# Optimization experiments

Hardware: AMD Instinct MI355X
Metric: run time of the kernel (lower is better)

Reference implementation:

```python
import jax, jax.numpy as jnp
import numpy as np
from jax import lax

C = 768
CA = C // 4  # adapter_channels = 192
L = 197      # 1 CLS + 14*14 patches
T_FRAMES = 16
B = 16
N = B * T_FRAMES


def quick_gelu(x):
    return x * jax.nn.sigmoid(1.702 * x)


def setup_inputs() -> dict:
    key = jax.random.key(0)
    ks = jax.random.split(key, 16)
    s = 0.02
    return {
        "x": jax.random.normal(ks[0], (L, N, C), dtype=jnp.float32),
        "T": T_FRAMES,
        # main path (fc1 -> depthwise conv1d over T -> fc2)
        "fc1_w": jax.random.normal(ks[1], (C, CA), jnp.float32) * s,
        "fc1_b": jnp.zeros((CA,), jnp.float32),
        "conv_w": jax.random.normal(ks[2], (CA, 1, 3), jnp.float32) * s,  # (O, I/g, K)
        "conv_b": jnp.zeros((CA,), jnp.float32),
        "fc2_w": jax.random.normal(ks[3], (CA, C), jnp.float32) * s,
        "fc2_b": jnp.zeros((C,), jnp.float32),
        # offset adapter (fc1 -> depthwise conv3d (1,3,3) -> fc2)
        "off_fc1_w": jax.random.normal(ks[4], (C, CA), jnp.float32) * s,
        "off_fc1_b": jnp.zeros((CA,), jnp.float32),
        "off_conv_w": jax.random.normal(ks[5], (CA, 1, 1, 3, 3), jnp.float32) * s,  # (O, I/g, D, H, W)
        "off_conv_b": jnp.zeros((CA,), jnp.float32),
        "off_fc2_w": jax.random.normal(ks[6], (CA, C), jnp.float32) * s,
        "off_fc2_b": jnp.zeros((C,), jnp.float32),
        # mlp branch (c_in -> QuickGELU -> c_out)
        "mlp_in_w": jax.random.normal(ks[7], (C, CA), jnp.float32) * s,
        "mlp_in_b": jnp.zeros((CA,), jnp.float32),
        "mlp_out_w": jax.random.normal(ks[8], (CA, C), jnp.float32) * s,
        "mlp_out_b": jnp.zeros((C,), jnp.float32),
    }


def _offset_adapter(x, T, fc1_w, fc1_b, conv_w, conv_b, fc2_w, fc2_b):
    Lx, Nx, Cx = x.shape
    Bx = Nx // T
    HW = Lx - 1
    H = int(round(HW ** 0.5))
    Ca = fc1_w.shape[1]
    xp = jnp.transpose(x, (1, 0, 2))            # (N, L, C)
    xs = xp[:, 1:, :].reshape(Bx, T, HW, Cx)    # (B, T, HW, C)
    # former frame: index [0, 0, 1, ..., T-2]
    x_former = jnp.concatenate([xs[:, :1], xs[:, :-1]], axis=1)
    off = xs - x_former
    off = off @ fc1_w + fc1_b                   # (B, T, HW, Ca)
    off = off.reshape(Bx, T, H, H, Ca).transpose(0, 4, 1, 2, 3)  # (B, Ca, T, H, W)
    off = lax.conv_general_dilated(
        off, conv_w, window_strides=(1, 1, 1),
        padding=[(0, 0), (1, 1), (1, 1)],
        dimension_numbers=("NCDHW", "OIDHW", "NCDHW"),
        feature_group_count=Ca,
    ) + conv_b[None, :, None, None, None]
    off = off.transpose(0, 2, 3, 4, 1).reshape(Nx, HW, Ca)
    off = off @ fc2_w + fc2_b                   # (N, L-1, C)
    return jnp.transpose(off, (1, 0, 2))        # (L-1, N, C)


def reference(x, T, fc1_w, fc1_b, conv_w, conv_b, fc2_w, fc2_b,
              off_fc1_w, off_fc1_b, off_conv_w, off_conv_b, off_fc2_w, off_fc2_b,
              mlp_in_w, mlp_in_b, mlp_out_w, mlp_out_b):
    Lx, Nx, Cx = x.shape
    Bx = Nx // T
    Ca = fc1_w.shape[1]

    offset = _offset_adapter(x, T, off_fc1_w, off_fc1_b, off_conv_w, off_conv_b,
                             off_fc2_w, off_fc2_b)  # (L-1, N, C)

    # mlp identity branch
    x_id = quick_gelu(x @ mlp_in_w + mlp_in_b) @ mlp_out_w + mlp_out_b  # (L, N, C)

    # main branch: fc1 -> depthwise conv1d along T -> fc2
    h = x @ fc1_w + fc1_b                                   # (L, N, Ca)
    h = jnp.transpose(h, (1, 0, 2)).reshape(Bx, T, Lx, Ca)  # (B, T, L, Ca)
    h = h.transpose(0, 2, 3, 1).reshape(Bx * Lx, Ca, T)     # (B*L, Ca, T)
    h = lax.conv_general_dilated(
        h, conv_w, window_strides=(1,), padding=[(1, 1)],
        dimension_numbers=("NCH", "OIH", "NCH"),
        feature_group_count=Ca,
    ) + conv_b[None, :, None]
    h = h.transpose(0, 2, 1).reshape(Bx, Lx, T, Ca)
    h = h.transpose(0, 2, 1, 3).reshape(Nx, Lx, Ca)
    h = jnp.transpose(h, (1, 0, 2))                         # (L, N, Ca)
    h = h @ fc2_w + fc2_b                                   # (L, N, C)

    x_id = x_id.at[1:].add(offset)
    return h + x_id
```

## Files before the change

### kernel.cpp

```cpp
#include <hip/hip_runtime.h>

#define L_DIM 197
#define N_DIM 256
#define C_DIM 768
#define CA_DIM 192
#define M_DIM (L_DIM * N_DIM)

typedef short s16x8 __attribute__((ext_vector_type(8)));
typedef float f32x4 __attribute__((ext_vector_type(4)));

__device__ __forceinline__ unsigned short f2bf(float f) {
  unsigned x = __builtin_bit_cast(unsigned, f);
  x = (x + 0x7fffu + ((x >> 16) & 1u)) >> 16;
  return (unsigned short)x;
}
__device__ __forceinline__ float bflo(unsigned u) { return __builtin_bit_cast(float, u << 16); }
__device__ __forceinline__ float bfhi(unsigned u) { return __builtin_bit_cast(float, u & 0xffff0000u); }

__device__ __forceinline__ void unp8(uint4 v, float* f) {
  f[0] = bflo(v.x); f[1] = bfhi(v.x); f[2] = bflo(v.y); f[3] = bfhi(v.y);
  f[4] = bflo(v.z); f[5] = bfhi(v.z); f[6] = bflo(v.w); f[7] = bfhi(v.w);
}

__device__ __forceinline__ unsigned cvtpk(float lo, float hi) {
  unsigned r;
  asm("v_cvt_pk_bf16_f32 %0, %1, %2" : "=v"(r) : "v"(lo), "v"(hi));
  return r;
}
__device__ __forceinline__ s16x8 cvt8(float4 p0, float4 p1) {
  uint4 u;
  u.x = cvtpk(p0.x, p0.y); u.y = cvtpk(p0.z, p0.w);
  u.z = cvtpk(p1.x, p1.y); u.w = cvtpk(p1.z, p1.w);
  return __builtin_bit_cast(s16x8, u);
}

__device__ __forceinline__ void mfma16(f32x4& acc, s16x8 a, s16x8 b) {
  asm("v_mfma_f32_16x16x32_bf16 %0, %1, %2, %0" : "+v"(acc) : "v"(a), "v"(b));
}

typedef const void __attribute__((address_space(1)))* gp_t;
typedef void __attribute__((address_space(3)))* lp_t;
__device__ __forceinline__ void gl16(const void* g, void* l) {
  __builtin_amdgcn_global_load_lds((gp_t)g, (lp_t)l, 16, 0, 0);
}

#define WAITVM(n) asm volatile("s_waitcnt vmcnt(" #n ")" ::: "memory")

__device__ __forceinline__ int swz(int pid, int nwg) {
  const int q = nwg >> 3, r = nwg & 7, x = pid & 7, s = pid >> 3;
  return (x < r ? x * (q + 1) : r * (q + 1) + (x - r) * q) + s;
}

__global__ __launch_bounds__(256) void prep_k(
    const float* __restrict__ fc1_w, const float* __restrict__ mlp_in_w,
    const float* __restrict__ off_fc1_w, const float* __restrict__ fc2_w,
    const float* __restrict__ mlp_out_w, const float* __restrict__ off_fc2_w,
    unsigned short* __restrict__ wa, unsigned short* __restrict__ wc) {
  __shared__ float t[32][33];
  const int b = blockIdx.x;
  const int job = b / 144, tt = b - job * 144;
  const float* in = job == 0 ? fc1_w : job == 1 ? mlp_in_w : job == 2 ? off_fc1_w
                  : job == 3 ? fc2_w : job == 4 ? mlp_out_w : off_fc2_w;
  const int Cc = job < 3 ? 192 : 768;
  const int tc = Cc >> 5;
  const int tr0 = (tt / tc) << 5, tc0 = (tt - (tt / tc) * tc) << 5;
  const int lr = threadIdx.x >> 5, lc = threadIdx.x & 31;
#pragma unroll
  for (int p = 0; p < 4; p++)
    t[p * 8 + lr][lc] = in[(tr0 + p * 8 + lr) * Cc + tc0 + lc];
  __syncthreads();
#pragma unroll
  for (int p = 0; p < 4; p++) {
    const int orow = tc0 + p * 8 + lr;
    const int ocol = tr0 + lc;
    const unsigned short v = f2bf(t[lc][p * 8 + lr]);
    if (job < 3) wa[(job * 192 + orow) * 768 + ocol] = v;
    else         wc[orow * 576 + (job - 3) * 192 + ocol] = v;
  }
}

__global__ __launch_bounds__(256, 1) void gemm_a_k(
    const float* __restrict__ x, const unsigned short* __restrict__ wa,
    const float* __restrict__ fc1_b, const float* __restrict__ mlp_in_b,
    const float* __restrict__ cw, const float* __restrict__ cb,
    const float* __restrict__ off_b1, unsigned short* __restrict__ hcat) {
  __shared__ float Asf[2][128 * 32];
  __shared__ unsigned short Bs[2][192 * 32];
  const int tid = threadIdx.x, lane = tid & 63, w = tid >> 6;
  const int lid = swz(blockIdx.x, 3 * 394);
  const int by = lid / 3, bx = lid - by * 3;
  const int m0 = by * 128, n0 = bx * 192;

  const int ar = tid >> 3, ac4 = (tid & 7) * 4;
  const float* gA = x + (size_t)(m0 + ar) * C_DIM + ac4;
  const int br = tid >> 2, bc8 = (tid & 3) * 8;
  const unsigned short* gB = wa + (size_t)(n0 + br) * C_DIM + bc8;

  auto stage = [&](int kt, int b) {
    const float* pa = gA + kt * 32;
#pragma unroll
    for (int j = 0; j < 4; j++)
      gl16(pa + (size_t)j * 32 * C_DIM, &Asf[b][(j * 32 + ar) * 32 + ac4]);
    const unsigned short* pb = gB + kt * 32;
#pragma unroll
    for (int j = 0; j < 3; j++)
      gl16(pb + (size_t)j * 64 * C_DIM, &Bs[b][(j * 64 + br) * 32 + bc8]);
  };

  f32x4 acc[4][6];
#pragma unroll
  for (int i = 0; i < 4; i++)
#pragma unroll
    for (int j = 0; j < 6; j++) acc[i][j] = (f32x4){0.f, 0.f, 0.f, 0.f};

  const int fr = lane & 15, fq = lane >> 4;
  const int wm = (w >> 1) * 64, wn = (w & 1) * 96;

  stage(0, 0);
  __syncthreads();
#pragma unroll 2
  for (int kt = 0; kt < 24; ++kt) {
    const int b = kt & 1;
    if (kt + 1 < 24) stage(kt + 1, b ^ 1);
    const float4* Af = (const float4*)&Asf[b][0];
    s16x8 af[4], bfv[6];
#pragma unroll
    for (int mi = 0; mi < 4; mi++) {
      const int row = wm + mi * 16 + fr;
      af[mi] = cvt8(Af[row * 8 + fq * 2], Af[row * 8 + fq * 2 + 1]);
    }
#pragma unroll
    for (int ni = 0; ni < 6; ni++)
      bfv[ni] = *(const s16x8*)&Bs[b][(wn + ni * 16 + fr) * 32 + fq * 8];
#pragma unroll
    for (int mi = 0; mi < 4; mi++)
#pragma unroll
      for (int ni = 0; ni < 6; ni++) mfma16(acc[mi][ni], af[mi], bfv[ni]);
    __syncthreads();
  }

  if (bx == 0) {
#pragma unroll
    for (int ni = 0; ni < 6; ni++) {
      const int ca = wn + ni * 16 + fr;
      const float bv = fc1_b[ca];
      const float w0 = cw[ca * 3], w1 = cw[ca * 3 + 1], w2 = cw[ca * 3 + 2];
      const float cbv = cb[ca];
#pragma unroll
      for (int mi = 0; mi < 4; mi++) {
        const float v0 = acc[mi][ni][0] + bv, v1 = acc[mi][ni][1] + bv;
        const float v2 = acc[mi][ni][2] + bv, v3 = acc[mi][ni][3] + bv;
        const float pv3 = __shfl_up(v3, 16);
        const float nv0 = __shfl_down(v0, 16);
        const float p0 = fq > 0 ? pv3 : 0.f;
        const float n3 = fq < 3 ? nv0 : 0.f;
        const int mb = m0 + wm + mi * 16 + fq * 4;
        hcat[(size_t)(mb + 0) * 576 + ca] = f2bf(w0 * p0 + w1 * v0 + w2 * v1 + cbv);
        hcat[(size_t)(mb + 1) * 576 + ca] = f2bf(w0 * v0 + w1 * v1 + w2 * v2 + cbv);
        hcat[(size_t)(mb + 2) * 576 + ca] = f2bf(w0 * v1 + w1 * v2 + w2 * v3 + cbv);
        hcat[(size_t)(mb + 3) * 576 + ca] = f2bf(w0 * v2 + w1 * v3 + w2 * n3 + cbv);
      }
    }
  } else if (bx == 1) {
#pragma unroll
    for (int ni = 0; ni < 6; ni++) {
      const int ca = wn + ni * 16 + fr;
      const float bv = mlp_in_b[ca];
#pragma unroll
      for (int mi = 0; mi < 4; mi++)
#pragma unroll
        for (int r = 0; r < 4; r++) {
          const int m = m0 + wm + mi * 16 + fq * 4 + r;
          float v = acc[mi][ni][r] + bv;
          v = v / (1.f + __expf(-1.702f * v));
          hcat[(size_t)m * 576 + 192 + ca] = f2bf(v);
        }
    }
  } else {
    const bool zrow = (by < 2);
#pragma unroll
    for (int ni = 0; ni < 6; ni++) {
      const int ca = wn + ni * 16 + fr;
      const float bv = off_b1[ca];
#pragma unroll
      for (int mi = 0; mi < 4; mi++) {
        const float v0 = acc[mi][ni][0], v1 = acc[mi][ni][1];
        const float v2 = acc[mi][ni][2], v3 = acc[mi][ni][3];
        const float pv3 = __shfl_up(v3, 16);
        const int mb = m0 + wm + mi * 16 + fq * 4;
        const float o0 = (fq == 0) ? bv : (v0 - pv3 + bv);
        if (zrow) {
          hcat[(size_t)(mb + 0) * 576 + 384 + ca] = 0;
          hcat[(size_t)(mb + 1) * 576 + 384 + ca] = 0;
          hcat[(size_t)(mb + 2) * 576 + 384 + ca] = 0;
          hcat[(size_t)(mb + 3) * 576 + 384 + ca] = 0;
        } else {
          hcat[(size_t)(mb + 0) * 576 + 384 + ca] = f2bf(o0);
          hcat[(size_t)(mb + 1) * 576 + 384 + ca] = f2bf(v1 - v0 + bv);
          hcat[(size_t)(mb + 2) * 576 + 384 + ca] = f2bf(v2 - v1 + bv);
          hcat[(size_t)(mb + 3) * 576 + 384 + ca] = f2bf(v3 - v2 + bv);
        }
      }
    }
  }
}

__global__ __launch_bounds__(256) void conv3d_k(
    const float* __restrict__ w3, const float* __restrict__ b2,
    unsigned short* __restrict__ hcat) {
  __shared__ float ds[196 * 48];
  __shared__ float w3s[9 * 48];
  __shared__ float b2s[48];
  const int blk = blockIdx.x;
  const int n = blk >> 2, q = blk & 3;
  const int ch0 = q * 48;
  const int tid = threadIdx.x;

  for (int j = tid; j < 432; j += 256) {
    const int c = j / 9, tap = j % 9;
    w3s[tap * 48 + c] = w3[(ch0 + c) * 9 + tap];
  }
  if (tid < 48) b2s[tid] = b2[ch0 + tid];

  for (int j = tid; j < 196 * 6; j += 256) {
    const int hw = j / 6, ck = j % 6;
    float dv[8];
    unp8(*(const uint4*)(hcat + ((size_t)(1 + hw) * 256 + n) * 576 + 384 + ch0 + ck * 8), dv);
#pragma unroll
    for (int e = 0; e < 8; e++) ds[hw * 48 + ck * 8 + e] = dv[e];
  }
  __syncthreads();

  for (int j = tid; j < 196 * 6; j += 256) {
    const int hw = j / 6, ck = j % 6;
    const int i = hw / 14, j0 = hw - i * 14;
    float acc[8];
#pragma unroll
    for (int e = 0; e < 8; e++) acc[e] = b2s[ck * 8 + e];
#pragma unroll
    for (int di = 0; di < 3; di++) {
      const int ii = i + di - 1;
      if (ii < 0 || ii >= 14) continue;
#pragma unroll
      for (int dj = 0; dj < 3; dj++) {
        const int jc = j0 + dj - 1;
        if (jc < 0 || jc >= 14) continue;
        const float* dp = &ds[(ii * 14 + jc) * 48 + ck * 8];
        const float* wp = &w3s[(di * 3 + dj) * 48 + ck * 8];
#pragma unroll
        for (int e = 0; e < 8; e++) acc[e] += wp[e] * dp[e];
      }
    }
    unsigned o[4];
#pragma unroll
    for (int e = 0; e < 8; e += 2)
      o[e / 2] = (unsigned)f2bf(acc[e]) | ((unsigned)f2bf(acc[e + 1]) << 16);
    uint4 ov; ov.x = o[0]; ov.y = o[1]; ov.z = o[2]; ov.w = o[3];
    *(uint4*)(hcat + ((size_t)(1 + hw) * 256 + n) * 576 + 384 + ch0 + ck * 8) = ov;
  }
}

__global__ __launch_bounds__(256, 1) void gemm_c_k(
    const unsigned short* __restrict__ hcat, const unsigned short* __restrict__ wc,
    const float* __restrict__ fc2_b, const float* __restrict__ mlp_out_b,
    const float* __restrict__ off_fc2_b, float* __restrict__ out) {
  __shared__ unsigned short As[3][128 * 32];
  __shared__ unsigned short Bs[3][256 * 32];
  const int tid = threadIdx.x, lane = tid & 63, w = tid >> 6;
  const int lid = swz(blockIdx.x, 3 * 394);
  const int by = lid / 3, bx = lid - by * 3;
  const int m0 = by * 128, n0 = bx * 256;

  const int sr = tid >> 2, sc = (tid & 3) * 8;
  const unsigned short* gA = hcat + (size_t)(m0 + sr) * 576 + sc;
  const unsigned short* gB = wc + (size_t)(n0 + sr) * 576 + sc;
  auto stage = [&](int kt, int b) {
#pragma unroll
    for (int j = 0; j < 2; j++)
      gl16(gA + kt * 32 + j * 64 * 576, &As[b][(sr + j * 64) * 32 + sc]);
#pragma unroll
    for (int j = 0; j < 4; j++)
      gl16(gB + kt * 32 + j * 64 * 576, &Bs[b][(sr + j * 64) * 32 + sc]);
  };

  f32x4 acc[4][8];
#pragma unroll
  for (int i = 0; i < 4; i++)
#pragma unroll
    for (int j = 0; j < 8; j++) acc[i][j] = (f32x4){0.f, 0.f, 0.f, 0.f};

  const int fr = lane & 15, fq = lane >> 4;
  const int wm = (w >> 1) * 64, wn = (w & 1) * 128;

  stage(0, 0);
#pragma unroll 3
  for (int kt = 0; kt < 18; ++kt) {
    const int b = kt % 3;
    if (kt + 1 < 18) { stage(kt + 1, (kt + 1) % 3); WAITVM(6); }
    else             { WAITVM(0); }
    __builtin_amdgcn_s_barrier();
    asm volatile("" ::: "memory");
    s16x8 af[4], bfv[8];
#pragma unroll
    for (int mi = 0; mi < 4; mi++)
      af[mi] = *(const s16x8*)&As[b][(wm + mi * 16 + fr) * 32 + fq * 8];
#pragma unroll
    for (int ni = 0; ni < 8; ni++)
      bfv[ni] = *(const s16x8*)&Bs[b][(wn + ni * 16 + fr) * 32 + fq * 8];
#pragma unroll
    for (int mi = 0; mi < 4; mi++)
#pragma unroll
      for (int ni = 0; ni < 8; ni++) mfma16(acc[mi][ni], af[mi], bfv[ni]);
  }

  float bv[8];
#pragma unroll
  for (int ni = 0; ni < 8; ni++) {
    const int c = n0 + wn + ni * 16 + fr;
    bv[ni] = fc2_b[c] + mlp_out_b[c] + (by >= 2 ? off_fc2_b[c] : 0.f);
  }
#pragma unroll
  for (int mi = 0; mi < 4; mi++)
#pragma unroll
    for (int r = 0; r < 4; r++) {
      const int m = m0 + wm + mi * 16 + fq * 4 + r;
      float* op = out + (size_t)m * C_DIM + n0 + wn;
#pragma unroll
      for (int ni = 0; ni < 8; ni++) op[ni * 16 + fr] = acc[mi][ni][r] + bv[ni];
    }
}

extern "C" void kernel_launch(void* const* d_in, const int* in_sizes, int n_in,
                              void* d_out, int out_size, void* d_ws, size_t ws_size,
                              hipStream_t stream) {
  const float* x          = (const float*)d_in[0];
  const float* fc1_w      = (const float*)d_in[2];
  const float* fc1_b      = (const float*)d_in[3];
  const float* conv_w     = (const float*)d_in[4];
  const float* conv_b     = (const float*)d_in[5];
  const float* fc2_w      = (const float*)d_in[6];
  const float* fc2_b      = (const float*)d_in[7];
  const float* off_fc1_w  = (const float*)d_in[8];
  const float* off_fc1_b  = (const float*)d_in[9];
  const float* off_conv_w = (const float*)d_in[10];
  const float* off_conv_b = (const float*)d_in[11];
  const float* off_fc2_w  = (const float*)d_in[12];
  const float* off_fc2_b  = (const float*)d_in[13];
  const float* mlp_in_w   = (const float*)d_in[14];
  const float* mlp_in_b   = (const float*)d_in[15];
  const float* mlp_out_w  = (const float*)d_in[16];
  const float* mlp_out_b  = (const float*)d_in[17];
  float* out = (float*)d_out;

  char* ws = (char*)d_ws;
  unsigned short* hcat = (unsigned short*)(ws);
  unsigned short* wa   = (unsigned short*)(ws + (size_t)M_DIM * 576 * 2);
  unsigned short* wc   = wa + (size_t)576 * 768;

  prep_k<<<864, 256, 0, stream>>>(fc1_w, mlp_in_w, off_fc1_w, fc2_w, mlp_out_w,
                                  off_fc2_w, wa, wc);
  gemm_a_k<<<1182, 256, 0, stream>>>(x, wa, fc1_b, mlp_in_b, conv_w, conv_b,
                                     off_fc1_b, hcat);
  conv3d_k<<<1024, 256, 0, stream>>>(off_conv_w, off_conv_b, hcat);
  gemm_c_k<<<1182, 256, 0, stream>>>(hcat, wc, fc2_b, mlp_out_b, off_fc2_b, out);
}
```

Before: 211.0 us.

## Pre-convert x to bf16 and compute all three fc1 branches per block

Adds a separate pass that converts x to bf16 once. gemm_a_k now uses 64-row tiles that cover all 576 output columns (three adapters), so each x row is loaded once instead of three times and no per-k fp32-to-bf16 conversion is needed. The cost is an extra kernel with a bf16 copy of x written and read back, a larger weight tile in LDS, and more accumulators per wave, which may limit occupancy.

```diff
diff --git a/kernel.cpp b/kernel.cpp
--- a/kernel.cpp
+++ b/kernel.cpp
@@ -20,18 +20,6 @@
 __device__ __forceinline__ void unp8(uint4 v, float* f) {
   f[0] = bflo(v.x); f[1] = bfhi(v.x); f[2] = bflo(v.y); f[3] = bfhi(v.y);
   f[4] = bflo(v.z); f[5] = bfhi(v.z); f[6] = bflo(v.w); f[7] = bfhi(v.w);
-}
-
-__device__ __forceinline__ unsigned cvtpk(float lo, float hi) {
-  unsigned r;
-  asm("v_cvt_pk_bf16_f32 %0, %1, %2" : "=v"(r) : "v"(lo), "v"(hi));
-  return r;
-}
-__device__ __forceinline__ s16x8 cvt8(float4 p0, float4 p1) {
-  uint4 u;
-  u.x = cvtpk(p0.x, p0.y); u.y = cvtpk(p0.z, p0.w);
-  u.z = cvtpk(p1.x, p1.y); u.w = cvtpk(p1.z, p1.w);
-  return __builtin_bit_cast(s16x8, u);
 }
 
 __device__ __forceinline__ void mfma16(f32x4& acc, s16x8 a, s16x8 b) {
@@ -79,42 +67,52 @@
   }
 }
 
-__global__ __launch_bounds__(256, 1) void gemm_a_k(
-    const float* __restrict__ x, const unsigned short* __restrict__ wa,
+__global__ __launch_bounds__(256) void xcvt_k(const float* __restrict__ x,
+                                              unsigned short* __restrict__ xb) {
+  const int total8 = M_DIM * C_DIM / 8;
+  const int step = gridDim.x * 256;
+  for (int i = blockIdx.x * 256 + threadIdx.x; i < total8; i += step) {
+    const float4 a = *(const float4*)(x + (size_t)i * 8);
+    const float4 b = *(const float4*)(x + (size_t)i * 8 + 4);
+    s16x8 v;
+    v[0] = (short)f2bf(a.x); v[1] = (short)f2bf(a.y);
+    v[2] = (short)f2bf(a.z); v[3] = (short)f2bf(a.w);
+    v[4] = (short)f2bf(b.x); v[5] = (short)f2bf(b.y);
+    v[6] = (short)f2bf(b.z); v[7] = (short)f2bf(b.w);
+    *(s16x8*)(xb + (size_t)i * 8) = v;
+  }
+}
+
+__global__ __launch_bounds__(256, 2) void gemm_a_k(
+    const unsigned short* __restrict__ xb, const unsigned short* __restrict__ wa,
     const float* __restrict__ fc1_b, const float* __restrict__ mlp_in_b,
     const float* __restrict__ cw, const float* __restrict__ cb,
     const float* __restrict__ off_b1, unsigned short* __restrict__ hcat) {
-  __shared__ float Asf[2][128 * 32];
-  __shared__ unsigned short Bs[2][192 * 32];
+  __shared__ unsigned short As[2][64 * 32];
+  __shared__ unsigned short Bs[2][576 * 32];
   const int tid = threadIdx.x, lane = tid & 63, w = tid >> 6;
-  const int lid = swz(blockIdx.x, 3 * 394);
-  const int by = lid / 3, bx = lid - by * 3;
-  const int m0 = by * 128, n0 = bx * 192;
-
-  const int ar = tid >> 3, ac4 = (tid & 7) * 4;
-  const float* gA = x + (size_t)(m0 + ar) * C_DIM + ac4;
-  const int br = tid >> 2, bc8 = (tid & 3) * 8;
-  const unsigned short* gB = wa + (size_t)(n0 + br) * C_DIM + bc8;
+  const int m0 = blockIdx.x * 64;
+
+  const int sr = tid >> 2, sc = (tid & 3) * 8;
+  const unsigned short* gA = xb + (size_t)(m0 + sr) * C_DIM + sc;
+  const unsigned short* gB = wa + (size_t)sr * C_DIM + sc;
 
   auto stage = [&](int kt, int b) {
-    const float* pa = gA + kt * 32;
-#pragma unroll
-    for (int j = 0; j < 4; j++)
-      gl16(pa + (size_t)j * 32 * C_DIM, &Asf[b][(j * 32 + ar) * 32 + ac4]);
+    gl16(gA + kt * 32, &As[b][sr * 32 + sc]);
     const unsigned short* pb = gB + kt * 32;
 #pragma unroll
-    for (int j = 0; j < 3; j++)
-      gl16(pb + (size_t)j * 64 * C_DIM, &Bs[b][(j * 64 + br) * 32 + bc8]);
+    for (int j = 0; j < 9; j++)
+      gl16(pb + (size_t)j * 64 * C_DIM, &Bs[b][(j * 64 + sr) * 32 + sc]);
   };
 
-  f32x4 acc[4][6];
+  f32x4 acc[4][9];
 #pragma unroll
   for (int i = 0; i < 4; i++)
 #pragma unroll
-    for (int j = 0; j < 6; j++) acc[i][j] = (f32x4){0.f, 0.f, 0.f, 0.f};
+    for (int j = 0; j < 9; j++) acc[i][j] = (f32x4){0.f, 0.f, 0.f, 0.f};
 
   const int fr = lane & 15, fq = lane >> 4;
-  const int wm = (w >> 1) * 64, wn = (w & 1) * 96;
+  const int wn = w * 144;
 
   stage(0, 0);
   __syncthreads();
@@ -122,27 +120,26 @@
   for (int kt = 0; kt < 24; ++kt) {
     const int b = kt & 1;
     if (kt + 1 < 24) stage(kt + 1, b ^ 1);
-    const float4* Af = (const float4*)&Asf[b][0];
-    s16x8 af[4], bfv[6];
-#pragma unroll
-    for (int mi = 0; mi < 4; mi++) {
-      const int row = wm + mi * 16 + fr;
-      af[mi] = cvt8(Af[row * 8 + fq * 2], Af[row * 8 + fq * 2 + 1]);
+    s16x8 af[4];
+#pragma unroll
+    for (int mi = 0; mi < 4; mi++)
+      af[mi] = *(const s16x8*)&As[b][(mi * 16 + fr) * 32 + fq * 8];
+#pragma unroll
+    for (int ni = 0; ni < 9; ni++) {
+      const s16x8 bf_ = *(const s16x8*)&Bs[b][(wn + ni * 16 + fr) * 32 + fq * 8];
+#pragma unroll
+      for (int mi = 0; mi < 4; mi++) mfma16(acc[mi][ni], af[mi], bf_);
     }
-#pragma unroll
-    for (int ni = 0; ni < 6; ni++)
-      bfv[ni] = *(const s16x8*)&Bs[b][(wn + ni * 16 + fr) * 32 + fq * 8];
-#pragma unroll
-    for (int mi = 0; mi < 4; mi++)
-#pragma unroll
-      for (int ni = 0; ni < 6; ni++) mfma16(acc[mi][ni], af[mi], bfv[ni]);
     __syncthreads();
   }
 
-  if (bx == 0) {
-#pragma unroll
-    for (int ni = 0; ni < 6; ni++) {
-      const int ca = wn + ni * 16 + fr;
+  const bool zrow = (m0 < 256);
+#pragma unroll
+  for (int ni = 0; ni < 9; ni++) {
+    const int cb_ = wn + ni * 16;
+    const int path = cb_ / 192;
+    const int ca = cb_ % 192 + fr;
+    if (path == 0) {
       const float bv = fc1_b[ca];
       const float w0 = cw[ca * 3], w1 = cw[ca * 3 + 1], w2 = cw[ca * 3 + 2];
       const float cbv = cb[ca];
@@ -154,40 +151,31 @@
         const float nv0 = __shfl_down(v0, 16);
         const float p0 = fq > 0 ? pv3 : 0.f;
         const float n3 = fq < 3 ? nv0 : 0.f;
-        const int mb = m0 + wm + mi * 16 + fq * 4;
+        const int mb = m0 + mi * 16 + fq * 4;
         hcat[(size_t)(mb + 0) * 576 + ca] = f2bf(w0 * p0 + w1 * v0 + w2 * v1 + cbv);
         hcat[(size_t)(mb + 1) * 576 + ca] = f2bf(w0 * v0 + w1 * v1 + w2 * v2 + cbv);
         hcat[(size_t)(mb + 2) * 576 + ca] = f2bf(w0 * v1 + w1 * v2 + w2 * v3 + cbv);
         hcat[(size_t)(mb + 3) * 576 + ca] = f2bf(w0 * v2 + w1 * v3 + w2 * n3 + cbv);
       }
-    }
-  } else if (bx == 1) {
-#pragma unroll
-    for (int ni = 0; ni < 6; ni++) {
-      const int ca = wn + ni * 16 + fr;
+    } else if (path == 1) {
       const float bv = mlp_in_b[ca];
 #pragma unroll
       for (int mi = 0; mi < 4; mi++)
 #pragma unroll
         for (int r = 0; r < 4; r++) {
-          const int m = m0 + wm + mi * 16 + fq * 4 + r;
+          const int m = m0 + mi * 16 + fq * 4 + r;
           float v = acc[mi][ni][r] + bv;
           v = v / (1.f + __expf(-1.702f * v));
           hcat[(size_t)m * 576 + 192 + ca] = f2bf(v);
         }
-    }
-  } else {
-    const bool zrow = (by < 2);
-#pragma unroll
-    for (int ni = 0; ni < 6; ni++) {
-      const int ca = wn + ni * 16 + fr;
+    } else {
       const float bv = off_b1[ca];
 #pragma unroll
       for (int mi = 0; mi < 4; mi++) {
         const float v0 = acc[mi][ni][0], v1 = acc[mi][ni][1];
         const float v2 = acc[mi][ni][2], v3 = acc[mi][ni][3];
         const float pv3 = __shfl_up(v3, 16);
-        const int mb = m0 + wm + mi * 16 + fq * 4;
+        const int mb = m0 + mi * 16 + fq * 4;
         const float o0 = (fq == 0) ? bv : (v0 - pv3 + bv);
         if (zrow) {
           hcat[(size_t)(mb + 0) * 576 + 384 + ca] = 0;
@@ -353,14 +341,17 @@
   float* out = (float*)d_out;
 
   char* ws = (char*)d_ws;
-  unsigned short* hcat = (unsigned short*)(ws);
-  unsigned short* wa   = (unsigned short*)(ws + (size_t)M_DIM * 576 * 2);
+  unsigned short* xb   = (unsigned short*)(ws);
+  unsigned short* hcat = (unsigned short*)(ws + (size_t)M_DIM * C_DIM * 2);
+  unsigned short* wa   = (unsigned short*)(ws + (size_t)M_DIM * C_DIM * 2
+                                              + (size_t)M_DIM * 576 * 2);
   unsigned short* wc   = wa + (size_t)576 * 768;
 
   prep_k<<<864, 256, 0, stream>>>(fc1_w, mlp_in_w, off_fc1_w, fc2_w, mlp_out_w,
                                   off_fc2_w, wa, wc);
-  gemm_a_k<<<1182, 256, 0, stream>>>(x, wa, fc1_b, mlp_in_b, conv_w, conv_b,
-                                     off_fc1_b, hcat);
+  xcvt_k<<<2048, 256, 0, stream>>>(x, xb);
+  gemm_a_k<<<788, 256, 0, stream>>>(xb, wa, fc1_b, mlp_in_b, conv_w, conv_b,
+                                    off_fc1_b, hcat);
   conv3d_k<<<1024, 256, 0, stream>>>(off_conv_w, off_conv_b, hcat);
   gemm_c_k<<<1182, 256, 0, stream>>>(hcat, wc, fc2_b, mlp_out_b, off_fc2_b, out);
 }
```

Result: slower. 228.8 us (+8.4%).

## Load A operand directly into registers and raise occupancy in fused GEMM-A

Applied to the files above, without the earlier changes.

The first GEMM stops staging the fp32 activation tile through shared memory. Each lane now loads its MFMA fragment rows straight from global into registers, one k-step ahead. B is still double-buffered in LDS via async loads, and the full __syncthreads is replaced with a vmcnt wait plus a raw barrier. Launch bounds now request 2 blocks per CU, which the smaller LDS footprint allows; the costs are more register pressure and less coalesced global reads for A, which is also re-read by the three column blocks.

```diff
diff --git a/kernel.cpp b/kernel.cpp
--- a/kernel.cpp
+++ b/kernel.cpp
@@ -79,56 +79,61 @@
   }
 }
 
-__global__ __launch_bounds__(256, 1) void gemm_a_k(
+__global__ __launch_bounds__(256, 2) void gemm_a_k(
     const float* __restrict__ x, const unsigned short* __restrict__ wa,
     const float* __restrict__ fc1_b, const float* __restrict__ mlp_in_b,
     const float* __restrict__ cw, const float* __restrict__ cb,
     const float* __restrict__ off_b1, unsigned short* __restrict__ hcat) {
-  __shared__ float Asf[2][128 * 32];
   __shared__ unsigned short Bs[2][192 * 32];
   const int tid = threadIdx.x, lane = tid & 63, w = tid >> 6;
   const int lid = swz(blockIdx.x, 3 * 394);
   const int by = lid / 3, bx = lid - by * 3;
   const int m0 = by * 128, n0 = bx * 192;
 
-  const int ar = tid >> 3, ac4 = (tid & 7) * 4;
-  const float* gA = x + (size_t)(m0 + ar) * C_DIM + ac4;
-  const int br = tid >> 2, bc8 = (tid & 3) * 8;
-  const unsigned short* gB = wa + (size_t)(n0 + br) * C_DIM + bc8;
-
-  auto stage = [&](int kt, int b) {
-    const float* pa = gA + kt * 32;
-#pragma unroll
-    for (int j = 0; j < 4; j++)
-      gl16(pa + (size_t)j * 32 * C_DIM, &Asf[b][(j * 32 + ar) * 32 + ac4]);
-    const unsigned short* pb = gB + kt * 32;
-#pragma unroll
-    for (int j = 0; j < 3; j++)
-      gl16(pb + (size_t)j * 64 * C_DIM, &Bs[b][(j * 64 + br) * 32 + bc8]);
-  };
-
-  f32x4 acc[4][6];
-#pragma unroll
-  for (int i = 0; i < 4; i++)
-#pragma unroll
-    for (int j = 0; j < 6; j++) acc[i][j] = (f32x4){0.f, 0.f, 0.f, 0.f};
-
   const int fr = lane & 15, fq = lane >> 4;
   const int wm = (w >> 1) * 64, wn = (w & 1) * 96;
 
-  stage(0, 0);
-  __syncthreads();
-#pragma unroll 2
+  const int sr = tid >> 2, sc = (tid & 3) * 8;
+  const unsigned short* gB = wa + (size_t)(n0 + sr) * C_DIM + sc;
+  auto stageB = [&](int kt, int b) {
+    const unsigned short* pb = gB + kt * 32;
+    gl16(pb,               &Bs[b][sr * 32 + sc]);
+    gl16(pb + 64 * C_DIM,  &Bs[b][(64 + sr) * 32 + sc]);
+    gl16(pb + 128 * C_DIM, &Bs[b][(128 + sr) * 32 + sc]);
+  };
+
+  float4 ar[8];
+  auto ldA = [&](int kt) {
+#pragma unroll
+    for (int mi = 0; mi < 4; mi++) {
+      const float* p = x + (size_t)(m0 + wm + mi * 16 + fr) * C_DIM + kt * 32 + fq * 8;
+      ar[2 * mi]     = *(const float4*)p;
+      ar[2 * mi + 1] = *(const float4*)(p + 4);
+    }
+  };
+
+  f32x4 acc[4][6];
+#pragma unroll
+  for (int i = 0; i < 4; i++)
+#pragma unroll
+    for (int j = 0; j < 6; j++) acc[i][j] = (f32x4){0.f, 0.f, 0.f, 0.f};
+
+  stageB(0, 0);
+  ldA(0);
+  WAITVM(8);
+  __builtin_amdgcn_s_barrier();
+  asm volatile("" ::: "memory");
+
   for (int kt = 0; kt < 24; ++kt) {
     const int b = kt & 1;
-    if (kt + 1 < 24) stage(kt + 1, b ^ 1);
-    const float4* Af = (const float4*)&Asf[b][0];
-    s16x8 af[4], bfv[6];
-#pragma unroll
-    for (int mi = 0; mi < 4; mi++) {
-      const int row = wm + mi * 16 + fr;
-      af[mi] = cvt8(Af[row * 8 + fq * 2], Af[row * 8 + fq * 2 + 1]);
-    }
+    s16x8 af[4];
+#pragma unroll
+    for (int mi = 0; mi < 4; mi++) af[mi] = cvt8(ar[2 * mi], ar[2 * mi + 1]);
+    if (kt + 1 < 24) {
+      stageB(kt + 1, b ^ 1);
+      ldA(kt + 1);
+    }
+    s16x8 bfv[6];
 #pragma unroll
     for (int ni = 0; ni < 6; ni++)
       bfv[ni] = *(const s16x8*)&Bs[b][(wn + ni * 16 + fr) * 32 + fq * 8];
@@ -136,7 +141,11 @@
     for (int mi = 0; mi < 4; mi++)
 #pragma unroll
       for (int ni = 0; ni < 6; ni++) mfma16(acc[mi][ni], af[mi], bfv[ni]);
-    __syncthreads();
+    if (kt + 1 < 24) {
+      WAITVM(8);
+      __builtin_amdgcn_s_barrier();
+      asm volatile("" ::: "memory");
+    }
   }
 
   if (bx == 0) {
```

Result: slower. 253.9 us (+20.4%).

## Pre-convert activations to bf16 in prep kernel and feed bf16 A tiles to GEMM

Applied to the files above, without the earlier changes.

Adds a grid-stride pass to the weight-prep kernel that converts all of x from fp32 to bf16 into a new workspace buffer. The first GEMM then loads bf16 A tiles directly with global_load_lds, so it no longer converts A inside the k-loop and needs half the LDS for A. Launch bounds are raised to allow three blocks per CU. The cost is an extra full read of x plus a bf16 write and re-read, and a larger workspace.

```diff
diff --git a/kernel.cpp b/kernel.cpp
--- a/kernel.cpp
+++ b/kernel.cpp
@@ -22,18 +22,6 @@
   f[4] = bflo(v.z); f[5] = bfhi(v.z); f[6] = bflo(v.w); f[7] = bfhi(v.w);
 }
 
-__device__ __forceinline__ unsigned cvtpk(float lo, float hi) {
-  unsigned r;
-  asm("v_cvt_pk_bf16_f32 %0, %1, %2" : "=v"(r) : "v"(lo), "v"(hi));
-  return r;
-}
-__device__ __forceinline__ s16x8 cvt8(float4 p0, float4 p1) {
-  uint4 u;
-  u.x = cvtpk(p0.x, p0.y); u.y = cvtpk(p0.z, p0.w);
-  u.z = cvtpk(p1.x, p1.y); u.w = cvtpk(p1.z, p1.w);
-  return __builtin_bit_cast(s16x8, u);
-}
-
 __device__ __forceinline__ void mfma16(f32x4& acc, s16x8 a, s16x8 b) {
   asm("v_mfma_f32_16x16x32_bf16 %0, %1, %2, %0" : "+v"(acc) : "v"(a), "v"(b));
 }
@@ -51,60 +39,75 @@
   return (x < r ? x * (q + 1) : r * (q + 1) + (x - r) * q) + s;
 }
 
-__global__ __launch_bounds__(256) void prep_k(
+__global__ __launch_bounds__(256) void prep_xcvt_k(
     const float* __restrict__ fc1_w, const float* __restrict__ mlp_in_w,
     const float* __restrict__ off_fc1_w, const float* __restrict__ fc2_w,
     const float* __restrict__ mlp_out_w, const float* __restrict__ off_fc2_w,
-    unsigned short* __restrict__ wa, unsigned short* __restrict__ wc) {
+    const float* __restrict__ x,
+    unsigned short* __restrict__ wa, unsigned short* __restrict__ wc,
+    unsigned short* __restrict__ xb) {
   __shared__ float t[32][33];
   const int b = blockIdx.x;
-  const int job = b / 144, tt = b - job * 144;
-  const float* in = job == 0 ? fc1_w : job == 1 ? mlp_in_w : job == 2 ? off_fc1_w
-                  : job == 3 ? fc2_w : job == 4 ? mlp_out_w : off_fc2_w;
-  const int Cc = job < 3 ? 192 : 768;
-  const int tc = Cc >> 5;
-  const int tr0 = (tt / tc) << 5, tc0 = (tt - (tt / tc) * tc) << 5;
-  const int lr = threadIdx.x >> 5, lc = threadIdx.x & 31;
-#pragma unroll
-  for (int p = 0; p < 4; p++)
-    t[p * 8 + lr][lc] = in[(tr0 + p * 8 + lr) * Cc + tc0 + lc];
-  __syncthreads();
-#pragma unroll
-  for (int p = 0; p < 4; p++) {
-    const int orow = tc0 + p * 8 + lr;
-    const int ocol = tr0 + lc;
-    const unsigned short v = f2bf(t[lc][p * 8 + lr]);
-    if (job < 3) wa[(job * 192 + orow) * 768 + ocol] = v;
-    else         wc[orow * 576 + (job - 3) * 192 + ocol] = v;
-  }
-}
-
-__global__ __launch_bounds__(256, 1) void gemm_a_k(
-    const float* __restrict__ x, const unsigned short* __restrict__ wa,
+  if (b < 864) {
+    const int job = b / 144, tt = b - job * 144;
+    const float* in = job == 0 ? fc1_w : job == 1 ? mlp_in_w : job == 2 ? off_fc1_w
+                    : job == 3 ? fc2_w : job == 4 ? mlp_out_w : off_fc2_w;
+    const int Cc = job < 3 ? 192 : 768;
+    const int tc = Cc >> 5;
+    const int tr0 = (tt / tc) << 5, tc0 = (tt - (tt / tc) * tc) << 5;
+    const int lr = threadIdx.x >> 5, lc = threadIdx.x & 31;
+#pragma unroll
+    for (int p = 0; p < 4; p++)
+      t[p * 8 + lr][lc] = in[(tr0 + p * 8 + lr) * Cc + tc0 + lc];
+    __syncthreads();
+#pragma unroll
+    for (int p = 0; p < 4; p++) {
+      const int orow = tc0 + p * 8 + lr;
+      const int ocol = tr0 + lc;
+      const unsigned short v = f2bf(t[lc][p * 8 + lr]);
+      if (job < 3) wa[(job * 192 + orow) * 768 + ocol] = v;
+      else         wc[orow * 576 + (job - 3) * 192 + ocol] = v;
+    }
+  } else {
+    const int total8 = M_DIM * C_DIM / 8;
+    const int step = 2048 * 256;
+    for (int i = (b - 864) * 256 + threadIdx.x; i < total8; i += step) {
+      const float4 a = *(const float4*)(x + (size_t)i * 8);
+      const float4 c = *(const float4*)(x + (size_t)i * 8 + 4);
+      s16x8 v;
+      v[0] = (short)f2bf(a.x); v[1] = (short)f2bf(a.y);
+      v[2] = (short)f2bf(a.z); v[3] = (short)f2bf(a.w);
+      v[4] = (short)f2bf(c.x); v[5] = (short)f2bf(c.y);
+      v[6] = (short)f2bf(c.z); v[7] = (short)f2bf(c.w);
+      *(s16x8*)(xb + (size_t)i * 8) = v;
+    }
+  }
+}
+
+__global__ __launch_bounds__(256, 3) void gemm_a_k(
+    const unsigned short* __restrict__ xb, const unsigned short* __restrict__ wa,
     const float* __restrict__ fc1_b, const float* __restrict__ mlp_in_b,
     const float* __restrict__ cw, const float* __restrict__ cb,
     const float* __restrict__ off_b1, unsigned short* __restrict__ hcat) {
-  __shared__ float Asf[2][128 * 32];
+  __shared__ unsigned short As[2][128 * 32];
   __shared__ unsigned short Bs[2][192 * 32];
   const int tid = threadIdx.x, lane = tid & 63, w = tid >> 6;
   const int lid = swz(blockIdx.x, 3 * 394);
   const int by = lid / 3, bx = lid - by * 3;
   const int m0 = by * 128, n0 = bx * 192;
 
-  const int ar = tid >> 3, ac4 = (tid & 7) * 4;
-  const float* gA = x + (size_t)(m0 + ar) * C_DIM + ac4;
-  const int br = tid >> 2, bc8 = (tid & 3) * 8;
-  const unsigned short* gB = wa + (size_t)(n0 + br) * C_DIM + bc8;
+  const int sr = tid >> 2, sc = (tid & 3) * 8;
+  const unsigned short* gA0 = xb + (size_t)(m0 + sr) * C_DIM + sc;
+  const unsigned short* gA1 = xb + (size_t)(m0 + 64 + sr) * C_DIM + sc;
+  const unsigned short* gB = wa + (size_t)(n0 + sr) * C_DIM + sc;
 
   auto stage = [&](int kt, int b) {
-    const float* pa = gA + kt * 32;
-#pragma unroll
-    for (int j = 0; j < 4; j++)
-      gl16(pa + (size_t)j * 32 * C_DIM, &Asf[b][(j * 32 + ar) * 32 + ac4]);
+    gl16(gA0 + kt * 32, &As[b][sr * 32 + sc]);
+    gl16(gA1 + kt * 32, &As[b][(64 + sr) * 32 + sc]);
     const unsigned short* pb = gB + kt * 32;
-#pragma unroll
-    for (int j = 0; j < 3; j++)
-      gl16(pb + (size_t)j * 64 * C_DIM, &Bs[b][(j * 64 + br) * 32 + bc8]);
+    gl16(pb,               &Bs[b][sr * 32 + sc]);
+    gl16(pb + 64 * C_DIM,  &Bs[b][(64 + sr) * 32 + sc]);
+    gl16(pb + 128 * C_DIM, &Bs[b][(128 + sr) * 32 + sc]);
   };
 
   f32x4 acc[4][6];
@@ -122,13 +125,10 @@
   for (int kt = 0; kt < 24; ++kt) {
     const int b = kt & 1;
     if (kt + 1 < 24) stage(kt + 1, b ^ 1);
-    const float4* Af = (const float4*)&Asf[b][0];
     s16x8 af[4], bfv[6];
 #pragma unroll
-    for (int mi = 0; mi < 4; mi++) {
-      const int row = wm + mi * 16 + fr;
-      af[mi] = cvt8(Af[row * 8 + fq * 2], Af[row * 8 + fq * 2 + 1]);
-    }
+    for (int mi = 0; mi < 4; mi++)
+      af[mi] = *(const s16x8*)&As[b][(wm + mi * 16 + fr) * 32 + fq * 8];
 #pragma unroll
     for (int ni = 0; ni < 6; ni++)
       bfv[ni] = *(const s16x8*)&Bs[b][(wn + ni * 16 + fr) * 32 + fq * 8];
@@ -353,13 +353,15 @@
   float* out = (float*)d_out;
 
   char* ws = (char*)d_ws;
-  unsigned short* hcat = (unsigned short*)(ws);
-  unsigned short* wa   = (unsigned short*)(ws + (size_t)M_DIM * 576 * 2);
+  unsigned short* xb   = (unsigned short*)(ws);
+  unsigned short* hcat = (unsigned short*)(ws + (size_t)M_DIM * C_DIM * 2);
+  unsigned short* wa   = (unsigned short*)(ws + (size_t)M_DIM * C_DIM * 2
+                                              + (size_t)M_DIM * 576 * 2);
   unsigned short* wc   = wa + (size_t)576 * 768;
 
-  prep_k<<<864, 256, 0, stream>>>(fc1_w, mlp_in_w, off_fc1_w, fc2_w, mlp_out_w,
-                                  off_fc2_w, wa, wc);
-  gemm_a_k<<<1182, 256, 0, stream>>>(x, wa, fc1_b, mlp_in_b, conv_w, conv_b,
+  prep_xcvt_k<<<2912, 256, 0, stream>>>(fc1_w, mlp_in_w, off_fc1_w, fc2_w,
+                                        mlp_out_w, off_fc2_w, x, wa, wc, xb);
+  gemm_a_k<<<1182, 256, 0, stream>>>(xb, wa, fc1_b, mlp_in_b, conv_w, conv_b,
                                      off_fc1_b, hcat);
   conv3d_k<<<1024, 256, 0, stream>>>(off_conv_w, off_conv_b, hcat);
   gemm_c_k<<<1182, 256, 0, stream>>>(hcat, wc, fc2_b, mlp_out_b, off_fc2_b, out);
```

Result: faster. 206.4 us (-2.1%).
